# Performance work log

Hardware: AMD Instinct MI355X
Metric: run time of the kernel (lower is better)

The kernel has to match this reference:

```python
import jax, jax.numpy as jnp
import numpy as np

B, D, H = 2048, 32, 512  # batch, state dim (x has D+1 cols incl. logdet slot), MLP hidden


def setup_inputs() -> dict:
    key = jax.random.key(0)
    ks = jax.random.split(key, 6)
    return {
        "t": jax.random.uniform(ks[0], (1,), dtype=jnp.float32),
        "x": jax.random.normal(ks[1], (B, D + 1), dtype=jnp.float32),
        "W1": jax.random.normal(ks[2], (D + 1, H), dtype=jnp.float32) / np.float32(np.sqrt(D + 1)),
        "b1": jnp.zeros((H,), jnp.float32),
        "W2": jax.random.normal(ks[3], (H, H), dtype=jnp.float32) / np.float32(np.sqrt(H)),
        "b2": jnp.zeros((H,), jnp.float32),
        "W3": jax.random.normal(ks[4], (H, D), dtype=jnp.float32) / np.float32(np.sqrt(H)),
        "b3": jnp.zeros((D,), jnp.float32),
    }


def _vf_single(xi, t, W1, b1, W2, b2, W3, b3):
    # single-sample vector field: R^D -> R^D, time t concatenated as a feature
    inp = jnp.concatenate([xi, t])  # (D+1,)
    h = jnp.tanh(inp @ W1 + b1)
    h = jnp.tanh(h @ W2 + b2)
    return h @ W3 + b3


def reference(t, x, W1, b1, W2, b2, W3, b3):
    xs = x[..., :-1]  # (B, D): drop logdet accumulator column
    # batched vector field dx = vf(t, xs)
    tt = jnp.broadcast_to(t, (xs.shape[0], 1))
    inp = jnp.concatenate([xs, tt], axis=-1)  # (B, D+1)
    h = jnp.tanh(inp @ W1 + b1)
    h = jnp.tanh(h @ W2 + b2)
    dx = h @ W3 + b3  # (B, D)
    # exact divergence: trace of per-sample Jacobian (torch vmap(jacrev) equivalent)
    f = lambda xi: _vf_single(xi, t, W1, b1, W2, b2, W3, b3)
    div = jax.vmap(lambda xi: jnp.trace(jax.jacfwd(f)(xi)))(xs)  # (B,)
    return jnp.concatenate([dx, div[:, None]], axis=-1)  # (B, D+1)
```

## Files before the change

kernel.cpp:

```cpp
#include <hip/hip_runtime.h>
#include <math.h>

constexpr int NB = 2048;
constexpr int ND = 32;
constexpr int NH = 512;
constexpr int NKI = NH / 32;

typedef __bf16 bf16x8 __attribute__((ext_vector_type(8)));
typedef float floatx4 __attribute__((ext_vector_type(4)));

__device__ inline float fast_tanh(float x) {
  float e = __expf(2.f * x);
  return 1.f - 2.f / (e + 1.f);
}


__global__ __launch_bounds__(256) void k_pre(
    const float* __restrict__ W1, const float* __restrict__ W2,
    const float* __restrict__ W3, __bf16* __restrict__ W2p,
    __bf16* __restrict__ Mp, float* __restrict__ W3T,
    __bf16* __restrict__ W1p, float* __restrict__ out) {
  int g = blockIdx.x * 256 + threadIdx.x;
  for (int idx = g; idx < NB * (ND + 1); idx += 65536) out[idx] = 0.f;
  if (g < ND * NH)
    W3T[g] = W3[(g & (NH - 1)) * ND + (g >> 9)];
  if (g < 4096) {
    int lane1 = g & 63;
    int ki1 = (g >> 6) & 1;
    int ct1 = g >> 7;
    int n1 = ct1 * 16 + (lane1 & 15);
    int k0 = ki1 * 32 + (lane1 >> 4) * 8;
    __bf16 v[8];
#pragma unroll
    for (int j = 0; j < 8; ++j) {
      int k = k0 + j;
      v[j] = (k <= ND) ? (__bf16)W1[k * NH + n1] : (__bf16)0.f;
    }
    *(bf16x8*)(W1p + (long)g * 8) = *(bf16x8*)v;
  }

  bool doM = blockIdx.x >= 128;
  int gid = (blockIdx.x & 127) * 256 + threadIdx.x;
  int lane = gid & 63;
  int ki = (gid >> 6) & (NKI - 1);
  int ct = gid >> 10;
  int n = ct * 16 + (lane & 15);
  int k0 = ki * 32 + (lane >> 4) * 8;
  long off = (long)gid * 8;

  if (!doM) {
    __bf16 v[8];
#pragma unroll
    for (int j = 0; j < 8; ++j) v[j] = (__bf16)W2[(k0 + j) * NH + n];
    *(bf16x8*)(W2p + off) = *(bf16x8*)v;
  } else {
    float acc[8];
#pragma unroll
    for (int j = 0; j < 8; ++j) acc[j] = 0.f;
    for (int i = 0; i < ND; ++i) {
      float w3 = W3[n * ND + i];
      float4 u = *(const float4*)&W1[i * NH + k0];
      float4 v = *(const float4*)&W1[i * NH + k0 + 4];
      acc[0] += w3 * u.x; acc[1] += w3 * u.y;
      acc[2] += w3 * u.z; acc[3] += w3 * u.w;
      acc[4] += w3 * v.x; acc[5] += w3 * v.y;
      acc[6] += w3 * v.z; acc[7] += w3 * v.w;
    }
    __bf16 v[8];
#pragma unroll
    for (int j = 0; j < 8; ++j)
      v[j] = (__bf16)(W2[(k0 + j) * NH + n] * acc[j]);
    *(bf16x8*)(Mp + off) = *(bf16x8*)v;
  }
}

__global__ __launch_bounds__(256) void k_main(
    const float* __restrict__ x, const float* __restrict__ t,
    const __bf16* __restrict__ W1p, const float* __restrict__ b1,
    const __bf16* __restrict__ W2p, const __bf16* __restrict__ Mp,
    const float* __restrict__ b2, const float* __restrict__ W3T,
    const float* __restrict__ b3, float* __restrict__ out) {
  __shared__ __bf16 xf[2 * 2 * 64 * 8];
  __shared__ __bf16 aH[2 * 16 * 64 * 8];
  __shared__ __bf16 aD[2 * 16 * 64 * 8];
  __shared__ float h2s[32][132];
  __shared__ float divred[4][32];

  int bid = blockIdx.x;
  int rb = bid >> 2;
  int q = bid & 3;
  int tid = threadIdx.x;
  int w = tid >> 6, lane = tid & 63;
  int col = lane & 15, quad = lane >> 4;
  float tv = t[0];

  {
    int lane0 = tid & 63;
    int ki0 = (tid >> 6) & 1;
    int rt0 = tid >> 7;
    int row = rb * 32 + rt0 * 16 + (lane0 & 15);
    int k0 = ki0 * 32 + (lane0 >> 4) * 8;
    __bf16 v[8];
#pragma unroll
    for (int j = 0; j < 8; ++j) {
      int k = k0 + j;
      float val = (k < ND) ? x[(long)row * (ND + 1) + k] : (k == ND ? tv : 0.f);
      v[j] = (__bf16)val;
    }
    *(bf16x8*)(xf + (long)tid * 8) = *(bf16x8*)v;
  }
  __syncthreads();

  {
    bf16x8 xa[2][2];
#pragma unroll
    for (int rt = 0; rt < 2; ++rt)
#pragma unroll
      for (int ki = 0; ki < 2; ++ki)
        xa[rt][ki] = *(const bf16x8*)(xf + ((rt * 2 + ki) * 64 + lane) * 8);
#pragma unroll 2
    for (int c8 = 0; c8 < 8; ++c8) {
      int ct1 = w * 8 + c8;
      floatx4 ac0 = {0, 0, 0, 0}, ac1 = {0, 0, 0, 0};
#pragma unroll
      for (int ki = 0; ki < 2; ++ki) {
        bf16x8 bw = *(const bf16x8*)(W1p + ((long)(ct1 * 2 + ki) * 64 + lane) * 8);
        ac0 = __builtin_amdgcn_mfma_f32_16x16x32_bf16(xa[0][ki], bw, ac0, 0, 0, 0);
        ac1 = __builtin_amdgcn_mfma_f32_16x16x32_bf16(xa[1][ki], bw, ac1, 0, 0, 0);
      }
      int n = ct1 * 16 + col;
      float bb = b1[n];
      int kio = n >> 5, hi = (n >> 3) & 3, j = n & 7;
#pragma unroll
      for (int rt = 0; rt < 2; ++rt) {
        floatx4 a = rt ? ac1 : ac0;
#pragma unroll
        for (int r = 0; r < 4; ++r) {
          float h = fast_tanh(a[r] + bb);
          int lanep = (quad * 4 + r) | (hi << 4);
          int ofs = ((rt * 16 + kio) * 64 + lanep) * 8 + j;
          aH[ofs] = (__bf16)h;
          aD[ofs] = (__bf16)(1.f - h * h);
        }
      }
    }
  }
  __syncthreads();

  int ct0 = q * 8 + w * 2;
  floatx4 accH[2][2] = {{{0,0,0,0},{0,0,0,0}},{{0,0,0,0},{0,0,0,0}}};
  floatx4 accM[2][2] = {{{0,0,0,0},{0,0,0,0}},{{0,0,0,0},{0,0,0,0}}};
#pragma unroll 2
  for (int ki = 0; ki < NKI; ++ki) {
    bf16x8 ah0 = *(const bf16x8*)(aH + ((0 * 16 + ki) * 64 + lane) * 8);
    bf16x8 ah1 = *(const bf16x8*)(aH + ((1 * 16 + ki) * 64 + lane) * 8);
    bf16x8 ad0 = *(const bf16x8*)(aD + ((0 * 16 + ki) * 64 + lane) * 8);
    bf16x8 ad1 = *(const bf16x8*)(aD + ((1 * 16 + ki) * 64 + lane) * 8);
#pragma unroll
    for (int cc = 0; cc < 2; ++cc) {
      long boff = ((long)((ct0 + cc) * NKI + ki) * 64 + lane) * 8;
      bf16x8 bw = *(const bf16x8*)(W2p + boff);
      bf16x8 bm = *(const bf16x8*)(Mp + boff);
      accH[0][cc] = __builtin_amdgcn_mfma_f32_16x16x32_bf16(ah0, bw, accH[0][cc], 0, 0, 0);
      accH[1][cc] = __builtin_amdgcn_mfma_f32_16x16x32_bf16(ah1, bw, accH[1][cc], 0, 0, 0);
      accM[0][cc] = __builtin_amdgcn_mfma_f32_16x16x32_bf16(ad0, bm, accM[0][cc], 0, 0, 0);
      accM[1][cc] = __builtin_amdgcn_mfma_f32_16x16x32_bf16(ad1, bm, accM[1][cc], 0, 0, 0);
    }
  }

  float divv[2][4] = {{0, 0, 0, 0}, {0, 0, 0, 0}};
#pragma unroll
  for (int cc = 0; cc < 2; ++cc) {
    int n = (ct0 + cc) * 16 + col;
    int nc = (w * 2 + cc) * 16 + col;
    float bb = b2[n];
#pragma unroll
    for (int rt = 0; rt < 2; ++rt) {
#pragma unroll
      for (int r = 0; r < 4; ++r) {
        float h2 = fast_tanh(accH[rt][cc][r] + bb);
        h2s[rt * 16 + quad * 4 + r][nc] = h2;
        divv[rt][r] += accM[rt][cc][r] * (1.f - h2 * h2);
      }
    }
  }
#pragma unroll
  for (int rt = 0; rt < 2; ++rt) {
#pragma unroll
    for (int r = 0; r < 4; ++r) {
      float v = divv[rt][r];
      v += __shfl_xor(v, 1);
      v += __shfl_xor(v, 2);
      v += __shfl_xor(v, 4);
      v += __shfl_xor(v, 8);
      if (col == 0) divred[w][rt * 16 + quad * 4 + r] = v;
    }
  }
  __syncthreads();
  if (tid < 32) {
    float v = divred[0][tid] + divred[1][tid] + divred[2][tid] + divred[3][tid];
    atomicAdd(&out[(long)(rb * 32 + tid) * (ND + 1) + ND], v);
  }

  int row = tid & 31;
  int i0 = tid >> 5;
  float a4[4] = {0.f, 0.f, 0.f, 0.f};
#pragma unroll 2
  for (int kk = 0; kk < 128; kk += 4) {
    float4 h = *(const float4*)&h2s[row][kk];
#pragma unroll
    for (int ii = 0; ii < 4; ++ii) {
      float4 wv = *(const float4*)&W3T[(long)(i0 * 4 + ii) * NH + q * 128 + kk];
      a4[ii] += h.x * wv.x + h.y * wv.y + h.z * wv.z + h.w * wv.w;
    }
  }
  float* orow = out + (long)(rb * 32 + row) * (ND + 1);
#pragma unroll
  for (int ii = 0; ii < 4; ++ii) {
    float v = a4[ii] + (q == 0 ? b3[i0 * 4 + ii] : 0.f);
    atomicAdd(&orow[i0 * 4 + ii], v);
  }
}

extern "C" void kernel_launch(void* const* d_in, const int* in_sizes, int n_in,
                              void* d_out, int out_size, void* d_ws, size_t ws_size,
                              hipStream_t stream) {
  const float* t  = (const float*)d_in[0];
  const float* x  = (const float*)d_in[1];
  const float* W1 = (const float*)d_in[2];
  const float* b1 = (const float*)d_in[3];
  const float* W2 = (const float*)d_in[4];
  const float* b2 = (const float*)d_in[5];
  const float* W3 = (const float*)d_in[6];
  const float* b3 = (const float*)d_in[7];
  float* out = (float*)d_out;

  __bf16* W2p = (__bf16*)d_ws;
  __bf16* Mp  = W2p + NH * NH;
  float*  W3T = (float*)(Mp + NH * NH);
  __bf16* W1p = (__bf16*)(W3T + ND * NH);

  k_pre<<<256, 256, 0, stream>>>(W1, W2, W3, W2p, Mp, W3T, W1p, out);
  k_main<<<256, 256, 0, stream>>>(x, t, W1p, b1, W2p, Mp, b2, W3T, b3, out);
}
```

Before: 103.0 us.

## Split hidden columns across 8 blocks per row tile and rebalance precompute

```diff
diff --git a/kernel.cpp b/kernel.cpp
--- a/kernel.cpp
+++ b/kernel.cpp
@@ -7,6 +7,7 @@
 constexpr int NKI = NH / 32;
 
 typedef __bf16 bf16x8 __attribute__((ext_vector_type(8)));
+typedef __bf16 bf16x4 __attribute__((ext_vector_type(4)));
 typedef float floatx4 __attribute__((ext_vector_type(4)));
 
 __device__ inline float fast_tanh(float x) {
@@ -39,38 +40,32 @@
     *(bf16x8*)(W1p + (long)g * 8) = *(bf16x8*)v;
   }
 
-  bool doM = blockIdx.x >= 128;
-  int gid = (blockIdx.x & 127) * 256 + threadIdx.x;
-  int lane = gid & 63;
-  int ki = (gid >> 6) & (NKI - 1);
-  int ct = gid >> 10;
+  int e = g * 4;
+  int lane = (e >> 3) & 63;
+  int ki = (e >> 9) & (NKI - 1);
+  int ct = e >> 13;
   int n = ct * 16 + (lane & 15);
-  int k0 = ki * 32 + (lane >> 4) * 8;
-  long off = (long)gid * 8;
-
-  if (!doM) {
-    __bf16 v[8];
-#pragma unroll
-    for (int j = 0; j < 8; ++j) v[j] = (__bf16)W2[(k0 + j) * NH + n];
-    *(bf16x8*)(W2p + off) = *(bf16x8*)v;
-  } else {
-    float acc[8];
-#pragma unroll
-    for (int j = 0; j < 8; ++j) acc[j] = 0.f;
+  int kb = ki * 32 + (lane >> 4) * 8 + (e & 4);
+
+  {
+    __bf16 v[4];
+#pragma unroll
+    for (int j = 0; j < 4; ++j) v[j] = (__bf16)W2[(kb + j) * NH + n];
+    *(bf16x4*)(W2p + e) = *(bf16x4*)v;
+  }
+  {
+    float acc[4] = {0.f, 0.f, 0.f, 0.f};
     for (int i = 0; i < ND; ++i) {
       float w3 = W3[n * ND + i];
-      float4 u = *(const float4*)&W1[i * NH + k0];
-      float4 v = *(const float4*)&W1[i * NH + k0 + 4];
+      float4 u = *(const float4*)&W1[i * NH + kb];
       acc[0] += w3 * u.x; acc[1] += w3 * u.y;
       acc[2] += w3 * u.z; acc[3] += w3 * u.w;
-      acc[4] += w3 * v.x; acc[5] += w3 * v.y;
-      acc[6] += w3 * v.z; acc[7] += w3 * v.w;
-    }
-    __bf16 v[8];
-#pragma unroll
-    for (int j = 0; j < 8; ++j)
-      v[j] = (__bf16)(W2[(k0 + j) * NH + n] * acc[j]);
-    *(bf16x8*)(Mp + off) = *(bf16x8*)v;
+    }
+    __bf16 v[4];
+#pragma unroll
+    for (int j = 0; j < 4; ++j)
+      v[j] = (__bf16)(W2[(kb + j) * NH + n] * acc[j]);
+    *(bf16x4*)(Mp + e) = *(bf16x4*)v;
   }
 }
 
@@ -83,12 +78,12 @@
   __shared__ __bf16 xf[2 * 2 * 64 * 8];
   __shared__ __bf16 aH[2 * 16 * 64 * 8];
   __shared__ __bf16 aD[2 * 16 * 64 * 8];
-  __shared__ float h2s[32][132];
+  __shared__ float h2s[32][68];
   __shared__ float divred[4][32];
 
   int bid = blockIdx.x;
-  int rb = bid >> 2;
-  int q = bid & 3;
+  int rb = bid >> 3;
+  int q = bid & 7;
   int tid = threadIdx.x;
   int w = tid >> 6, lane = tid & 63;
   int col = lane & 15, quad = lane >> 4;
@@ -147,40 +142,36 @@
   }
   __syncthreads();
 
-  int ct0 = q * 8 + w * 2;
-  floatx4 accH[2][2] = {{{0,0,0,0},{0,0,0,0}},{{0,0,0,0},{0,0,0,0}}};
-  floatx4 accM[2][2] = {{{0,0,0,0},{0,0,0,0}},{{0,0,0,0},{0,0,0,0}}};
-#pragma unroll 2
+  int ct0 = q * 4 + w;
+  floatx4 accH[2] = {{0,0,0,0},{0,0,0,0}};
+  floatx4 accM[2] = {{0,0,0,0},{0,0,0,0}};
+#pragma unroll 4
   for (int ki = 0; ki < NKI; ++ki) {
     bf16x8 ah0 = *(const bf16x8*)(aH + ((0 * 16 + ki) * 64 + lane) * 8);
     bf16x8 ah1 = *(const bf16x8*)(aH + ((1 * 16 + ki) * 64 + lane) * 8);
     bf16x8 ad0 = *(const bf16x8*)(aD + ((0 * 16 + ki) * 64 + lane) * 8);
     bf16x8 ad1 = *(const bf16x8*)(aD + ((1 * 16 + ki) * 64 + lane) * 8);
-#pragma unroll
-    for (int cc = 0; cc < 2; ++cc) {
-      long boff = ((long)((ct0 + cc) * NKI + ki) * 64 + lane) * 8;
-      bf16x8 bw = *(const bf16x8*)(W2p + boff);
-      bf16x8 bm = *(const bf16x8*)(Mp + boff);
-      accH[0][cc] = __builtin_amdgcn_mfma_f32_16x16x32_bf16(ah0, bw, accH[0][cc], 0, 0, 0);
-      accH[1][cc] = __builtin_amdgcn_mfma_f32_16x16x32_bf16(ah1, bw, accH[1][cc], 0, 0, 0);
-      accM[0][cc] = __builtin_amdgcn_mfma_f32_16x16x32_bf16(ad0, bm, accM[0][cc], 0, 0, 0);
-      accM[1][cc] = __builtin_amdgcn_mfma_f32_16x16x32_bf16(ad1, bm, accM[1][cc], 0, 0, 0);
-    }
+    long boff = ((long)(ct0 * NKI + ki) * 64 + lane) * 8;
+    bf16x8 bw = *(const bf16x8*)(W2p + boff);
+    bf16x8 bm = *(const bf16x8*)(Mp + boff);
+    accH[0] = __builtin_amdgcn_mfma_f32_16x16x32_bf16(ah0, bw, accH[0], 0, 0, 0);
+    accH[1] = __builtin_amdgcn_mfma_f32_16x16x32_bf16(ah1, bw, accH[1], 0, 0, 0);
+    accM[0] = __builtin_amdgcn_mfma_f32_16x16x32_bf16(ad0, bm, accM[0], 0, 0, 0);
+    accM[1] = __builtin_amdgcn_mfma_f32_16x16x32_bf16(ad1, bm, accM[1], 0, 0, 0);
   }
 
   float divv[2][4] = {{0, 0, 0, 0}, {0, 0, 0, 0}};
-#pragma unroll
-  for (int cc = 0; cc < 2; ++cc) {
-    int n = (ct0 + cc) * 16 + col;
-    int nc = (w * 2 + cc) * 16 + col;
+  {
+    int n = ct0 * 16 + col;
+    int nc = w * 16 + col;
     float bb = b2[n];
 #pragma unroll
     for (int rt = 0; rt < 2; ++rt) {
 #pragma unroll
       for (int r = 0; r < 4; ++r) {
-        float h2 = fast_tanh(accH[rt][cc][r] + bb);
+        float h2 = fast_tanh(accH[rt][r] + bb);
         h2s[rt * 16 + quad * 4 + r][nc] = h2;
-        divv[rt][r] += accM[rt][cc][r] * (1.f - h2 * h2);
+        divv[rt][r] += accM[rt][r] * (1.f - h2 * h2);
       }
     }
   }
@@ -205,12 +196,12 @@
   int row = tid & 31;
   int i0 = tid >> 5;
   float a4[4] = {0.f, 0.f, 0.f, 0.f};
-#pragma unroll 2
-  for (int kk = 0; kk < 128; kk += 4) {
+#pragma unroll 4
+  for (int kk = 0; kk < 64; kk += 4) {
     float4 h = *(const float4*)&h2s[row][kk];
 #pragma unroll
     for (int ii = 0; ii < 4; ++ii) {
-      float4 wv = *(const float4*)&W3T[(long)(i0 * 4 + ii) * NH + q * 128 + kk];
+      float4 wv = *(const float4*)&W3T[(long)(i0 * 4 + ii) * NH + q * 64 + kk];
       a4[ii] += h.x * wv.x + h.y * wv.y + h.z * wv.z + h.w * wv.w;
     }
   }
@@ -241,5 +232,5 @@
   __bf16* W1p = (__bf16*)(W3T + ND * NH);
 
   k_pre<<<256, 256, 0, stream>>>(W1, W2, W3, W2p, Mp, W3T, W1p, out);
-  k_main<<<256, 256, 0, stream>>>(x, t, W1p, b1, W2p, Mp, b2, W3T, b3, out);
-}
+  k_main<<<512, 256, 0, stream>>>(x, t, W1p, b1, W2p, Mp, b2, W3T, b3, out);
+}
```

After: 105.1 us. 1.02x slower.
